# Performance work log

Measured on AMD Instinct MI355X. Metric: run time of the kernel, lower is better.

The kernel has to match this reference:

```python
import math
import jax, jax.numpy as jnp
import numpy as np

BS, N, D, H = 4, 512, 1024, 16
HD = D // H


def setup_inputs() -> dict:
    key = jax.random.key(0)
    ks = jax.random.split(key, 12)
    s = 1.0 / math.sqrt(D)
    return {
        "x": jax.random.normal(ks[0], (BS, N, D), jnp.float32),
        "r": jax.random.normal(ks[1], (BS, 3, N, N), jnp.float32),
        "bias": jax.random.normal(ks[2], (BS, H, N, N), jnp.float32),
        "mask": jax.random.randint(ks[3], (BS, 1, N, N), 0, 2, jnp.int32),
        "wq": jax.random.normal(ks[4], (D, D), jnp.float32) * s,
        "bq": jnp.zeros((D,), jnp.float32),
        "wk": jax.random.normal(ks[5], (D, D), jnp.float32) * s,
        "bk": jnp.zeros((D,), jnp.float32),
        "wv": jax.random.normal(ks[6], (D, D), jnp.float32) * s,
        "bv": jnp.zeros((D,), jnp.float32),
        "wo": jax.random.normal(ks[7], (D, 1), jnp.float32) * s,
        "bo": jnp.zeros((1,), jnp.float32),
    }


def reference(x, r, bias, mask, wq, bq, wk, bk, wv, bv, wo, bo):
    bs, n, d = x.shape
    # projections -> (bs, h, n, hd)
    q = (x @ wq + bq).reshape(bs, n, H, HD).transpose(0, 2, 1, 3)
    k = (x @ wk + bk).reshape(bs, n, H, HD).transpose(0, 2, 1, 3)
    v = (x @ wv + bv).reshape(bs, n, H, HD).transpose(0, 2, 1, 3)
    logits = jnp.einsum("bhid,bhjd->bhij", q, k) / math.sqrt(HD) + bias
    logits = jnp.where(mask == 0, jnp.float32(-1e9), logits)
    w = jax.nn.softmax(logits, axis=-1)  # (bs,h,n,n)
    # o[b,i,c,h,d] = sum_j r[b,c,i,j] * w[b,h,i,j] * v[b,h,j,d]
    o = jnp.einsum("bcij,bhij,bhjd->bichd", r, w, v)
    o = o.reshape(bs, n, 3, d)
    force = o @ wo + bo  # (bs, n, 3, 1)
    return force
```

## Files before the change

### kernel.cpp

```cpp
#include <hip/hip_runtime.h>
#include <stdint.h>

#define BSZ 4
#define NSEQ 512
#define DMOD 1024
#define NH 16
#define HD 64

typedef __attribute__((ext_vector_type(8))) short bf16x8;
typedef __attribute__((ext_vector_type(4))) float f32x4;

__device__ __forceinline__ unsigned short f2bf(float f) {
    union { float f; uint32_t u; } v; v.f = f;
    uint32_t u = v.u;
    u += 0x7FFFu + ((u >> 16) & 1u);
    return (unsigned short)(u >> 16);
}

__device__ __forceinline__ void gload_lds16(const unsigned short* g, unsigned short* l) {
    __builtin_amdgcn_global_load_lds(
        (const __attribute__((address_space(1))) void*)g,
        (__attribute__((address_space(3))) void*)l, 16, 0, 0);
}

#define LGKM_BAR() do { \
    asm volatile("s_waitcnt lgkmcnt(0)" ::: "memory"); \
    __builtin_amdgcn_sched_barrier(0); \
    __builtin_amdgcn_s_barrier(); \
    __builtin_amdgcn_sched_barrier(0); } while (0)

__global__ __launch_bounds__(256) void k_prep(
        const float* __restrict__ x, const float* __restrict__ wq, const float* __restrict__ wk,
        const float* __restrict__ wv, const float* __restrict__ bv, const float* __restrict__ wo,
        unsigned short* __restrict__ xb, unsigned short* __restrict__ wqt,
        unsigned short* __restrict__ wkt, float* __restrict__ wv2t, float* __restrict__ bv2) {
    __shared__ float t[32][33];
    int bx = blockIdx.x, tid = threadIdx.x;
    if (bx < 2048) {
        int i = bx * 256 + tid;
        float4 v = ((const float4*)x)[i];
        ushort4 o; o.x = f2bf(v.x); o.y = f2bf(v.y); o.z = f2bf(v.z); o.w = f2bf(v.w);
        ((ushort4*)xb)[i] = o;
    } else if (bx < 4096) {
        int g = bx - 2048; int z = g >> 10; g &= 1023;
        const float* src = z ? wk : wq;
        unsigned short* dst = z ? wkt : wqt;
        int be = (g & 31) * 32, bc = (g >> 5) * 32;
        int tx = tid & 31, ty = tid >> 5;
        #pragma unroll
        for (int yy = 0; yy < 32; yy += 8)
            t[ty + yy][tx] = src[(size_t)(be + ty + yy) * DMOD + bc + tx];
        __syncthreads();
        #pragma unroll
        for (int yy = 0; yy < 32; yy += 8)
            dst[(size_t)(bc + ty + yy) * DMOD + be + tx] = f2bf(t[tx][ty + yy]);
    } else {
        int g = bx - 4096;
        int grp = tid >> 6, l = tid & 63;
        int e = g * 4 + grp;
        float out = 0.f;
        #pragma unroll
        for (int it = 0; it < 16; ++it) {
            float v = wv[(size_t)e * DMOD + it * 64 + l] * wo[it * 64 + l];
            #pragma unroll
            for (int off = 1; off < 64; off <<= 1) v += __shfl_xor(v, off, 64);
            if (l == it) out = v;
        }
        if (l < 16) wv2t[l * DMOD + e] = out;
        if (g == 0 && grp == 0) {
            float ob = 0.f;
            #pragma unroll
            for (int it = 0; it < 16; ++it) {
                float v = bv[it * 64 + l] * wo[it * 64 + l];
                #pragma unroll
                for (int off = 1; off < 64; off <<= 1) v += __shfl_xor(v, off, 64);
                if (l == it) ob = v;
            }
            if (l < 16) bv2[l] = ob;
        }
    }
}

__global__ __launch_bounds__(256, 3) void k_mid(
        const float* __restrict__ x, const float* __restrict__ wv2t, const float* __restrict__ bv2,
        const unsigned short* __restrict__ xb, const unsigned short* __restrict__ wqt,
        const unsigned short* __restrict__ wkt, const float* __restrict__ bq,
        const float* __restrict__ bk, float* __restrict__ u,
        unsigned short* __restrict__ qT, unsigned short* __restrict__ kT) {
    __shared__ unsigned short lA[128 * 64];
    __shared__ unsigned short lB[128 * 64];
    int bx = blockIdx.x, tid = threadIdx.x;
    if (bx >= 256) {
        int wave = (bx - 256) * 4 + (tid >> 6);
        int l = tid & 63;
        int b = wave >> 9, j = wave & 511;
        const float* xr = x + (size_t)(b * NSEQ + j) * DMOD;
        float p[16];
        #pragma unroll
        for (int h = 0; h < 16; ++h) p[h] = 0.f;
        for (int it = 0; it < 16; ++it) {
            int e = l + it * 64;
            float xv = xr[e];
            #pragma unroll
            for (int h = 0; h < 16; ++h) p[h] += xv * wv2t[h * DMOD + e];
        }
        #pragma unroll
        for (int h = 0; h < 16; ++h) {
            #pragma unroll
            for (int off = 1; off < 64; off <<= 1) p[h] += __shfl_xor(p[h], off, 64);
        }
        float out = 0.f;
        #pragma unroll
        for (int h = 0; h < 16; ++h) if (l == h) out = p[h] + bv2[h];
        if (l < 16) u[(b * 16 + l) * NSEQ + j] = out;
        return;
    }
    int g = bx;
    int mt = g & 15, nt8 = (g >> 4) & 7, z = g >> 7;
    const unsigned short* Wt = z ? wkt : wqt;
    const float* bias = z ? bk : bq;
    unsigned short* outT = z ? kT : qT;
    float scale = z ? 1.f : 0.125f;
    int m0 = mt * 128, n0 = nt8 * 128;
    int w = tid >> 6, lane = tid & 63;
    int wr = w >> 1, wc = w & 1;
    int quad = lane >> 4, cs = lane & 15;
    int l8 = lane >> 3, l7 = lane & 7;
    int sg = l7 ^ l8;

    f32x4 acc[4][4];
    #pragma unroll
    for (int mi = 0; mi < 4; ++mi)
        #pragma unroll
        for (int ni = 0; ni < 4; ++ni) acc[mi][ni] = (f32x4){0.f, 0.f, 0.f, 0.f};

    for (int kc = 0; kc < 16; ++kc) {
        int k0 = kc * 64;
        #pragma unroll
        for (int q = 0; q < 4; ++q) {
            int row = w * 32 + q * 8 + l8;
            gload_lds16(xb + (size_t)(m0 + row) * DMOD + k0 + sg * 8,
                        &lA[(w * 32 + q * 8) * 64]);
            gload_lds16(Wt + (size_t)(n0 + row) * DMOD + k0 + sg * 8,
                        &lB[(w * 32 + q * 8) * 64]);
        }
        __syncthreads();
        #pragma unroll
        for (int ks = 0; ks < 2; ++ks) {
            bf16x8 af[4], bfr[4];
            #pragma unroll
            for (int mi = 0; mi < 4; ++mi) {
                int row = wr * 64 + mi * 16 + cs;
                int gq = (ks * 4 + quad) ^ (row & 7);
                af[mi] = *(const bf16x8*)&lA[row * 64 + gq * 8];
            }
            #pragma unroll
            for (int ni = 0; ni < 4; ++ni) {
                int row = wc * 64 + ni * 16 + cs;
                int gq = (ks * 4 + quad) ^ (row & 7);
                bfr[ni] = *(const bf16x8*)&lB[row * 64 + gq * 8];
            }
            #pragma unroll
            for (int mi = 0; mi < 4; ++mi)
                #pragma unroll
                for (int ni = 0; ni < 4; ++ni)
                    acc[mi][ni] = __builtin_amdgcn_mfma_f32_16x16x32_bf16(
                        af[mi], bfr[ni], acc[mi][ni], 0, 0, 0);
        }
        __syncthreads();
    }
    #pragma unroll
    for (int ni = 0; ni < 4; ++ni) {
        int n = n0 + wc * 64 + ni * 16 + cs;
        int h = n >> 6, d = n & 63;
        float bvv = bias[n];
        #pragma unroll
        for (int mi = 0; mi < 4; ++mi) {
            #pragma unroll
            for (int rr = 0; rr < 4; ++rr) {
                int mg = m0 + wr * 64 + mi * 16 + quad * 4 + rr;
                int b = mg >> 9, i = mg & 511;
                outT[(size_t)((b * 16 + h) * NSEQ + i) * HD + d] =
                    f2bf((acc[mi][ni][rr] + bvv) * scale);
            }
        }
    }
}

__global__ __launch_bounds__(512, 4) void k_attn(
        const unsigned short* __restrict__ qT, const unsigned short* __restrict__ kT,
        const float* __restrict__ bias, const int* __restrict__ mask,
        const float* __restrict__ u, const float* __restrict__ r,
        float* __restrict__ spart, float* __restrict__ P) {
    __shared__ float rT4[16 * 64 * 4];
    int tid = threadIdx.x;
    int w = tid >> 6, lane = tid & 63;
    int quad = lane >> 4, col = lane & 15;
    int it = blockIdx.x, jc = blockIdx.y, b = blockIdx.z;
    int i0 = it * 16, j0 = jc * 64;

    float s0[2], s1[2], s2[2], smf[2];
    const float* rbase = r + (size_t)b * 3 * NSEQ * NSEQ;
    const int* mrow = mask + (size_t)b * NSEQ * NSEQ;
    #pragma unroll
    for (int t = 0; t < 2; ++t) {
        int slot = t * 512 + tid;
        int il = slot >> 6, jl = slot & 63;
        size_t off = (size_t)(i0 + il) * NSEQ + j0 + jl;
        s0[t] = rbase[off];
        s1[t] = rbase[(size_t)NSEQ * NSEQ + off];
        s2[t] = rbase[2 * (size_t)NSEQ * NSEQ + off];
        smf[t] = (float)mrow[off];
    }
    #pragma unroll
    for (int t = 0; t < 2; ++t) {
        int slot = t * 512 + tid;
        float4 pk; pk.x = s0[t]; pk.y = s1[t]; pk.z = s2[t]; pk.w = smf[t];
        *(float4*)&rT4[slot * 4] = pk;
    }

    LGKM_BAR();

    #pragma unroll
    for (int hg = 0; hg < 2; ++hg) {
        int bh = b * 16 + hg * 8 + w;

        const unsigned short* qbase = qT + ((size_t)(bh * NSEQ + i0 + col)) * HD + quad * 8;
        bf16x8 a0 = *(const bf16x8*)qbase;
        bf16x8 a1 = *(const bf16x8*)(qbase + 32);

        bf16x8 kf0[4], kf1[4];
        #pragma unroll
        for (int jt = 0; jt < 4; ++jt) {
            const unsigned short* kbase =
                kT + ((size_t)(bh * NSEQ + j0 + jt * 16 + col)) * HD + quad * 8;
            kf0[jt] = *(const bf16x8*)kbase;
            kf1[jt] = *(const bf16x8*)(kbase + 32);
        }
        const float* brow = bias + (size_t)bh * NSEQ * NSEQ;
        float bvv[16];
        #pragma unroll
        for (int jt = 0; jt < 4; ++jt) {
            int j = j0 + jt * 16 + col;
            #pragma unroll
            for (int rr = 0; rr < 4; ++rr) {
                int i = i0 + quad * 4 + rr;
                bvv[jt * 4 + rr] = __builtin_nontemporal_load(&brow[(size_t)i * NSEQ + j]);
            }
        }
        const float* ub = u + (size_t)bh * NSEQ;
        float uvv[4];
        #pragma unroll
        for (int jt = 0; jt < 4; ++jt) uvv[jt] = ub[j0 + jt * 16 + col];

        float sp[4] = {0.f, 0.f, 0.f, 0.f};
        float pc0[4] = {0.f, 0.f, 0.f, 0.f};
        float pc1[4] = {0.f, 0.f, 0.f, 0.f};
        float pc2[4] = {0.f, 0.f, 0.f, 0.f};
        #pragma unroll
        for (int jt = 0; jt < 4; ++jt) {
            f32x4 acc = (f32x4){0.f, 0.f, 0.f, 0.f};
            acc = __builtin_amdgcn_mfma_f32_16x16x32_bf16(a0, kf0[jt], acc, 0, 0, 0);
            acc = __builtin_amdgcn_mfma_f32_16x16x32_bf16(a1, kf1[jt], acc, 0, 0, 0);
            float uv = uvv[jt];
            int jl = jt * 16 + col;
            #pragma unroll
            for (int rr = 0; rr < 4; ++rr) {
                int il = quad * 4 + rr;
                float4 v = *(const float4*)&rT4[(il * 64 + jl) * 4];
                float lg = acc[rr] + bvv[jt * 4 + rr];
                float e = __expf(lg) * v.w;
                sp[rr] += e;
                float eu = e * uv;
                pc0[rr] += eu * v.x;
                pc1[rr] += eu * v.y;
                pc2[rr] += eu * v.z;
            }
        }
        #pragma unroll
        for (int rr = 0; rr < 4; ++rr) {
            #pragma unroll
            for (int off = 1; off < 16; off <<= 1) {
                sp[rr]  += __shfl_xor(sp[rr], off, 64);
                pc0[rr] += __shfl_xor(pc0[rr], off, 64);
                pc1[rr] += __shfl_xor(pc1[rr], off, 64);
                pc2[rr] += __shfl_xor(pc2[rr], off, 64);
            }
        }
        if (col == 0) {
            #pragma unroll
            for (int rr = 0; rr < 4; ++rr) {
                int il = quad * 4 + rr;
                spart[((size_t)bh * NSEQ + i0 + il) * 8 + jc] = sp[rr];
                size_t pb = ((((size_t)bh * 32 + it) * 16 + il) * 8 + jc) * 3;
                P[pb + 0] = pc0[rr];
                P[pb + 1] = pc1[rr];
                P[pb + 2] = pc2[rr];
            }
        }
    }
}

__global__ __launch_bounds__(256) void k_final(
        const float* __restrict__ spart, const float* __restrict__ P,
        const float* __restrict__ bo, float* __restrict__ out) {
    __shared__ float part[4][16][3];
    int bx = blockIdx.x;
    int b = bx >> 5, it = bx & 31;
    int tid = threadIdx.x;
    int il = tid & 15, h = tid >> 4;
    int w = tid >> 6;
    int bh = b * 16 + h;
    int i = it * 16 + il;
    const float* sprow = spart + ((size_t)bh * NSEQ + i) * 8;
    float4 sa = *(const float4*)sprow;
    float4 sb = *(const float4*)(sprow + 4);
    float s = sa.x + sa.y + sa.z + sa.w + sb.x + sb.y + sb.z + sb.w;
    float sinv = (s > 0.f) ? 1.f / s : 0.f;
    const float* pbase = P + (((size_t)bh * 32 + it) * 16 + il) * 24;
    float f[3] = {0.f, 0.f, 0.f};
    #pragma unroll
    for (int q = 0; q < 6; ++q) {
        float4 v = *(const float4*)(pbase + q * 4);
        f[(q * 4 + 0) % 3] += v.x;
        f[(q * 4 + 1) % 3] += v.y;
        f[(q * 4 + 2) % 3] += v.z;
        f[(q * 4 + 3) % 3] += v.w;
    }
    f[0] *= sinv; f[1] *= sinv; f[2] *= sinv;
    #pragma unroll
    for (int c = 0; c < 3; ++c) {
        f[c] += __shfl_xor(f[c], 16, 64);
        f[c] += __shfl_xor(f[c], 32, 64);
    }
    if ((tid & 48) == 0) {
        part[w][il][0] = f[0]; part[w][il][1] = f[1]; part[w][il][2] = f[2];
    }
    __syncthreads();
    if (tid < 16) {
        float bov = bo[0];
        float o0 = part[0][tid][0] + part[1][tid][0] + part[2][tid][0] + part[3][tid][0];
        float o1 = part[0][tid][1] + part[1][tid][1] + part[2][tid][1] + part[3][tid][1];
        float o2 = part[0][tid][2] + part[1][tid][2] + part[2][tid][2] + part[3][tid][2];
        size_t row = (size_t)b * NSEQ + it * 16 + tid;
        out[row * 3 + 0] = o0 + bov;
        out[row * 3 + 1] = o1 + bov;
        out[row * 3 + 2] = o2 + bov;
    }
}

extern "C" void kernel_launch(void* const* d_in, const int* in_sizes, int n_in,
                              void* d_out, int out_size, void* d_ws, size_t ws_size,
                              hipStream_t stream) {
    const float* x    = (const float*)d_in[0];
    const float* rr   = (const float*)d_in[1];
    const float* bias = (const float*)d_in[2];
    const int*   mask = (const int*)d_in[3];
    const float* wq   = (const float*)d_in[4];
    const float* bq   = (const float*)d_in[5];
    const float* wk   = (const float*)d_in[6];
    const float* bk   = (const float*)d_in[7];
    const float* wv   = (const float*)d_in[8];
    const float* bv   = (const float*)d_in[9];
    const float* wo   = (const float*)d_in[10];
    const float* bo   = (const float*)d_in[11];
    float* out = (float*)d_out;

    char* ws = (char*)d_ws;
    unsigned short* xb    = (unsigned short*)(ws + 0);
    unsigned short* wqt   = (unsigned short*)(ws + 4194304);
    unsigned short* wkt   = (unsigned short*)(ws + 6291456);
    float*          wv2t  = (float*)(ws + 8388608);
    float*          bv2   = (float*)(ws + 8454144);
    float*          u     = (float*)(ws + 8454400);
    unsigned short* qT    = (unsigned short*)(ws + 8585472);
    unsigned short* kT    = (unsigned short*)(ws + 12779776);
    float*          spart = (float*)(ws + 16974080);
    float*          P     = (float*)(ws + 18022656);

    k_prep<<<4352, 256, 0, stream>>>(x, wq, wk, wv, bv, wo, xb, wqt, wkt, wv2t, bv2);
    k_mid<<<768, 256, 0, stream>>>(x, wv2t, bv2, xb, wqt, wkt, bq, bk, u, qT, kT);
    k_attn<<<dim3(32, 8, 4), 512, 0, stream>>>(qT, kT, bias, mask, u, rr, spart, P);
    k_final<<<128, 256, 0, stream>>>(spart, P, bo, out);
}
```

Baseline: 194.7 us.

## Split attention heads across grid and stream bias tile into LDS asynchronously

```diff
diff --git a/kernel.cpp b/kernel.cpp
--- a/kernel.cpp
+++ b/kernel.cpp
@@ -18,6 +18,12 @@
 }
 
 __device__ __forceinline__ void gload_lds16(const unsigned short* g, unsigned short* l) {
+    __builtin_amdgcn_global_load_lds(
+        (const __attribute__((address_space(1))) void*)g,
+        (__attribute__((address_space(3))) void*)l, 16, 0, 0);
+}
+
+__device__ __forceinline__ void gload_lds16f(const float* g, float* l) {
     __builtin_amdgcn_global_load_lds(
         (const __attribute__((address_space(1))) void*)g,
         (__attribute__((address_space(3))) void*)l, 16, 0, 0);
@@ -187,17 +193,23 @@
     }
 }
 
+#define BGRP 264
+#define BHEAD 1056
 __global__ __launch_bounds__(512, 4) void k_attn(
         const unsigned short* __restrict__ qT, const unsigned short* __restrict__ kT,
         const float* __restrict__ bias, const int* __restrict__ mask,
         const float* __restrict__ u, const float* __restrict__ r,
         float* __restrict__ spart, float* __restrict__ P) {
+    __shared__ float bias_lds[8 * BHEAD];
     __shared__ float rT4[16 * 64 * 4];
     int tid = threadIdx.x;
     int w = tid >> 6, lane = tid & 63;
     int quad = lane >> 4, col = lane & 15;
-    int it = blockIdx.x, jc = blockIdx.y, b = blockIdx.z;
+    int it = blockIdx.x, jc = blockIdx.y, bz = blockIdx.z;
+    int b = bz >> 1, hg = bz & 1;
     int i0 = it * 16, j0 = jc * 64;
+    int h = hg * 8 + w;
+    int bh = b * 16 + h;
 
     float s0[2], s1[2], s2[2], smf[2];
     const float* rbase = r + (size_t)b * 3 * NSEQ * NSEQ;
@@ -212,6 +224,32 @@
         s2[t] = rbase[2 * (size_t)NSEQ * NSEQ + off];
         smf[t] = (float)mrow[off];
     }
+
+    const unsigned short* qbase = qT + ((size_t)(bh * NSEQ + i0 + col)) * HD + quad * 8;
+    bf16x8 a0 = *(const bf16x8*)qbase;
+    bf16x8 a1 = *(const bf16x8*)(qbase + 32);
+    bf16x8 kf0[4], kf1[4];
+    #pragma unroll
+    for (int jt = 0; jt < 4; ++jt) {
+        const unsigned short* kbase =
+            kT + ((size_t)(bh * NSEQ + j0 + jt * 16 + col)) * HD + quad * 8;
+        kf0[jt] = *(const bf16x8*)kbase;
+        kf1[jt] = *(const bf16x8*)(kbase + 32);
+    }
+    const float* ub = u + (size_t)bh * NSEQ;
+    float uvv[4];
+    #pragma unroll
+    for (int jt = 0; jt < 4; ++jt) uvv[jt] = ub[j0 + jt * 16 + col];
+
+    {
+        const float* bsrc = bias + (size_t)bh * NSEQ * NSEQ;
+        int il4 = lane >> 4, jl4 = (lane & 15) * 4;
+        #pragma unroll
+        for (int g = 0; g < 4; ++g)
+            gload_lds16f(bsrc + (size_t)(i0 + g * 4 + il4) * NSEQ + j0 + jl4,
+                         &bias_lds[w * BHEAD + g * BGRP]);
+    }
+
     #pragma unroll
     for (int t = 0; t < 2; ++t) {
         int slot = t * 512 + tid;
@@ -220,83 +258,54 @@
     }
 
     LGKM_BAR();
-
-    #pragma unroll
-    for (int hg = 0; hg < 2; ++hg) {
-        int bh = b * 16 + hg * 8 + w;
-
-        const unsigned short* qbase = qT + ((size_t)(bh * NSEQ + i0 + col)) * HD + quad * 8;
-        bf16x8 a0 = *(const bf16x8*)qbase;
-        bf16x8 a1 = *(const bf16x8*)(qbase + 32);
-
-        bf16x8 kf0[4], kf1[4];
-        #pragma unroll
-        for (int jt = 0; jt < 4; ++jt) {
-            const unsigned short* kbase =
-                kT + ((size_t)(bh * NSEQ + j0 + jt * 16 + col)) * HD + quad * 8;
-            kf0[jt] = *(const bf16x8*)kbase;
-            kf1[jt] = *(const bf16x8*)(kbase + 32);
-        }
-        const float* brow = bias + (size_t)bh * NSEQ * NSEQ;
-        float bvv[16];
-        #pragma unroll
-        for (int jt = 0; jt < 4; ++jt) {
-            int j = j0 + jt * 16 + col;
-            #pragma unroll
-            for (int rr = 0; rr < 4; ++rr) {
-                int i = i0 + quad * 4 + rr;
-                bvv[jt * 4 + rr] = __builtin_nontemporal_load(&brow[(size_t)i * NSEQ + j]);
-            }
-        }
-        const float* ub = u + (size_t)bh * NSEQ;
-        float uvv[4];
-        #pragma unroll
-        for (int jt = 0; jt < 4; ++jt) uvv[jt] = ub[j0 + jt * 16 + col];
-
-        float sp[4] = {0.f, 0.f, 0.f, 0.f};
-        float pc0[4] = {0.f, 0.f, 0.f, 0.f};
-        float pc1[4] = {0.f, 0.f, 0.f, 0.f};
-        float pc2[4] = {0.f, 0.f, 0.f, 0.f};
-        #pragma unroll
-        for (int jt = 0; jt < 4; ++jt) {
-            f32x4 acc = (f32x4){0.f, 0.f, 0.f, 0.f};
-            acc = __builtin_amdgcn_mfma_f32_16x16x32_bf16(a0, kf0[jt], acc, 0, 0, 0);
-            acc = __builtin_amdgcn_mfma_f32_16x16x32_bf16(a1, kf1[jt], acc, 0, 0, 0);
-            float uv = uvv[jt];
-            int jl = jt * 16 + col;
-            #pragma unroll
-            for (int rr = 0; rr < 4; ++rr) {
-                int il = quad * 4 + rr;
-                float4 v = *(const float4*)&rT4[(il * 64 + jl) * 4];
-                float lg = acc[rr] + bvv[jt * 4 + rr];
-                float e = __expf(lg) * v.w;
-                sp[rr] += e;
-                float eu = e * uv;
-                pc0[rr] += eu * v.x;
-                pc1[rr] += eu * v.y;
-                pc2[rr] += eu * v.z;
-            }
-        }
+    asm volatile("s_waitcnt vmcnt(0)" ::: "memory");
+    __builtin_amdgcn_sched_barrier(0);
+
+    const float* bwave = &bias_lds[w * BHEAD];
+    float sp[4] = {0.f, 0.f, 0.f, 0.f};
+    float pc0[4] = {0.f, 0.f, 0.f, 0.f};
+    float pc1[4] = {0.f, 0.f, 0.f, 0.f};
+    float pc2[4] = {0.f, 0.f, 0.f, 0.f};
+    #pragma unroll
+    for (int jt = 0; jt < 4; ++jt) {
+        f32x4 acc = (f32x4){0.f, 0.f, 0.f, 0.f};
+        acc = __builtin_amdgcn_mfma_f32_16x16x32_bf16(a0, kf0[jt], acc, 0, 0, 0);
+        acc = __builtin_amdgcn_mfma_f32_16x16x32_bf16(a1, kf1[jt], acc, 0, 0, 0);
+        float uv = uvv[jt];
+        int jl = jt * 16 + col;
         #pragma unroll
         for (int rr = 0; rr < 4; ++rr) {
-            #pragma unroll
-            for (int off = 1; off < 16; off <<= 1) {
-                sp[rr]  += __shfl_xor(sp[rr], off, 64);
-                pc0[rr] += __shfl_xor(pc0[rr], off, 64);
-                pc1[rr] += __shfl_xor(pc1[rr], off, 64);
-                pc2[rr] += __shfl_xor(pc2[rr], off, 64);
-            }
-        }
-        if (col == 0) {
-            #pragma unroll
-            for (int rr = 0; rr < 4; ++rr) {
-                int il = quad * 4 + rr;
-                spart[((size_t)bh * NSEQ + i0 + il) * 8 + jc] = sp[rr];
-                size_t pb = ((((size_t)bh * 32 + it) * 16 + il) * 8 + jc) * 3;
-                P[pb + 0] = pc0[rr];
-                P[pb + 1] = pc1[rr];
-                P[pb + 2] = pc2[rr];
-            }
+            int il = quad * 4 + rr;
+            float4 v = *(const float4*)&rT4[(il * 64 + jl) * 4];
+            float bvv = bwave[quad * BGRP + rr * 64 + jl];
+            float lg = acc[rr] + bvv;
+            float e = __expf(lg) * v.w;
+            sp[rr] += e;
+            float eu = e * uv;
+            pc0[rr] += eu * v.x;
+            pc1[rr] += eu * v.y;
+            pc2[rr] += eu * v.z;
+        }
+    }
+    #pragma unroll
+    for (int rr = 0; rr < 4; ++rr) {
+        #pragma unroll
+        for (int off = 1; off < 16; off <<= 1) {
+            sp[rr]  += __shfl_xor(sp[rr], off, 64);
+            pc0[rr] += __shfl_xor(pc0[rr], off, 64);
+            pc1[rr] += __shfl_xor(pc1[rr], off, 64);
+            pc2[rr] += __shfl_xor(pc2[rr], off, 64);
+        }
+    }
+    if (col == 0) {
+        #pragma unroll
+        for (int rr = 0; rr < 4; ++rr) {
+            int il = quad * 4 + rr;
+            spart[((size_t)bh * NSEQ + i0 + il) * 8 + jc] = sp[rr];
+            size_t pb = ((((size_t)bh * 32 + it) * 16 + il) * 8 + jc) * 3;
+            P[pb + 0] = pc0[rr];
+            P[pb + 1] = pc1[rr];
+            P[pb + 2] = pc2[rr];
         }
     }
 }
@@ -380,6 +389,6 @@
 
     k_prep<<<4352, 256, 0, stream>>>(x, wq, wk, wv, bv, wo, xb, wqt, wkt, wv2t, bv2);
     k_mid<<<768, 256, 0, stream>>>(x, wv2t, bv2, xb, wqt, wkt, bq, bk, u, qT, kT);
-    k_attn<<<dim3(32, 8, 4), 512, 0, stream>>>(qT, kT, bias, mask, u, rr, spart, P);
+    k_attn<<<dim3(32, 8, 8), 512, 0, stream>>>(qT, kT, bias, mask, u, rr, spart, P);
     k_final<<<128, 256, 0, stream>>>(spart, P, bo, out);
 }
```

After: 186.7 us. -4.1%, faster.

## Restructure attention kernel to loop over key chunks with double-buffered prefetch

Applied to the files above, without the earlier changes.

```diff
diff --git a/kernel.cpp b/kernel.cpp
--- a/kernel.cpp
+++ b/kernel.cpp
@@ -187,88 +187,96 @@
     }
 }
 
-__global__ __launch_bounds__(512, 4) void k_attn(
+__global__ __launch_bounds__(512, 2) void k_attn(
         const unsigned short* __restrict__ qT, const unsigned short* __restrict__ kT,
         const float* __restrict__ bias, const int* __restrict__ mask,
         const float* __restrict__ u, const float* __restrict__ r,
         float* __restrict__ spart, float* __restrict__ P) {
-    __shared__ float rT4[16 * 64 * 4];
+    __shared__ float rT4[2][16 * 64 * 4];
     int tid = threadIdx.x;
     int w = tid >> 6, lane = tid & 63;
     int quad = lane >> 4, col = lane & 15;
-    int it = blockIdx.x, jc = blockIdx.y, b = blockIdx.z;
-    int i0 = it * 16, j0 = jc * 64;
-
-    float s0[2], s1[2], s2[2], smf[2];
+    int it = blockIdx.x, bz = blockIdx.y;
+    int b = bz >> 1, hg = bz & 1;
+    int i0 = it * 16;
+    int h = hg * 8 + w;
+    int bh = b * 16 + h;
+
     const float* rbase = r + (size_t)b * 3 * NSEQ * NSEQ;
     const int* mrow = mask + (size_t)b * NSEQ * NSEQ;
-    #pragma unroll
-    for (int t = 0; t < 2; ++t) {
-        int slot = t * 512 + tid;
-        int il = slot >> 6, jl = slot & 63;
-        size_t off = (size_t)(i0 + il) * NSEQ + j0 + jl;
-        s0[t] = rbase[off];
-        s1[t] = rbase[(size_t)NSEQ * NSEQ + off];
-        s2[t] = rbase[2 * (size_t)NSEQ * NSEQ + off];
-        smf[t] = (float)mrow[off];
-    }
-    #pragma unroll
-    for (int t = 0; t < 2; ++t) {
-        int slot = t * 512 + tid;
-        float4 pk; pk.x = s0[t]; pk.y = s1[t]; pk.z = s2[t]; pk.w = smf[t];
-        *(float4*)&rT4[slot * 4] = pk;
-    }
-
-    LGKM_BAR();
-
-    #pragma unroll
-    for (int hg = 0; hg < 2; ++hg) {
-        int bh = b * 16 + hg * 8 + w;
-
-        const unsigned short* qbase = qT + ((size_t)(bh * NSEQ + i0 + col)) * HD + quad * 8;
-        bf16x8 a0 = *(const bf16x8*)qbase;
-        bf16x8 a1 = *(const bf16x8*)(qbase + 32);
-
-        bf16x8 kf0[4], kf1[4];
+    const float* brow = bias + (size_t)bh * NSEQ * NSEQ;
+    const unsigned short* kbh = kT + (size_t)bh * NSEQ * HD;
+    const float* ub = u + (size_t)bh * NSEQ;
+
+    const unsigned short* qbase = qT + ((size_t)(bh * NSEQ + i0 + col)) * HD + quad * 8;
+    bf16x8 a0 = *(const bf16x8*)qbase;
+    bf16x8 a1 = *(const bf16x8*)(qbase + 32);
+
+    bf16x8 kf0[2][4], kf1[2][4];
+    float uvv[2][4], bvv[2][16];
+    float s0[2][2], s1[2][2], s2[2][2], smf[2][2];
+
+    auto prefetch = [&](int jc, int pb) {
+        int j0 = jc * 64;
         #pragma unroll
         for (int jt = 0; jt < 4; ++jt) {
-            const unsigned short* kbase =
-                kT + ((size_t)(bh * NSEQ + j0 + jt * 16 + col)) * HD + quad * 8;
-            kf0[jt] = *(const bf16x8*)kbase;
-            kf1[jt] = *(const bf16x8*)(kbase + 32);
-        }
-        const float* brow = bias + (size_t)bh * NSEQ * NSEQ;
-        float bvv[16];
-        #pragma unroll
-        for (int jt = 0; jt < 4; ++jt) {
+            const unsigned short* kb = kbh + ((size_t)(j0 + jt * 16 + col)) * HD + quad * 8;
+            kf0[pb][jt] = *(const bf16x8*)kb;
+            kf1[pb][jt] = *(const bf16x8*)(kb + 32);
+            uvv[pb][jt] = ub[j0 + jt * 16 + col];
             int j = j0 + jt * 16 + col;
             #pragma unroll
             for (int rr = 0; rr < 4; ++rr) {
                 int i = i0 + quad * 4 + rr;
-                bvv[jt * 4 + rr] = __builtin_nontemporal_load(&brow[(size_t)i * NSEQ + j]);
-            }
-        }
-        const float* ub = u + (size_t)bh * NSEQ;
-        float uvv[4];
-        #pragma unroll
-        for (int jt = 0; jt < 4; ++jt) uvv[jt] = ub[j0 + jt * 16 + col];
-
-        float sp[4] = {0.f, 0.f, 0.f, 0.f};
+                bvv[pb][jt * 4 + rr] = __builtin_nontemporal_load(&brow[(size_t)i * NSEQ + j]);
+            }
+        }
+        #pragma unroll
+        for (int t = 0; t < 2; ++t) {
+            int slot = t * 512 + tid;
+            int il = slot >> 6, jl = slot & 63;
+            size_t off = (size_t)(i0 + il) * NSEQ + j0 + jl;
+            s0[pb][t] = rbase[off];
+            s1[pb][t] = rbase[(size_t)NSEQ * NSEQ + off];
+            s2[pb][t] = rbase[2 * (size_t)NSEQ * NSEQ + off];
+            smf[pb][t] = (float)mrow[off];
+        }
+    };
+    auto pack = [&](int pb) {
+        #pragma unroll
+        for (int t = 0; t < 2; ++t) {
+            int slot = t * 512 + tid;
+            float4 pk; pk.x = s0[pb][t]; pk.y = s1[pb][t]; pk.z = s2[pb][t]; pk.w = smf[pb][t];
+            *(float4*)&rT4[pb][slot * 4] = pk;
+        }
+    };
+
+    prefetch(0, 0);
+    pack(0);
+    LGKM_BAR();
+
+    #pragma unroll 8
+    for (int jc = 0; jc < 8; ++jc) {
+        int cur = jc & 1, nxt = cur ^ 1;
+        if (jc < 7) prefetch(jc + 1, nxt);
+
+        float sp[4]  = {0.f, 0.f, 0.f, 0.f};
         float pc0[4] = {0.f, 0.f, 0.f, 0.f};
         float pc1[4] = {0.f, 0.f, 0.f, 0.f};
         float pc2[4] = {0.f, 0.f, 0.f, 0.f};
+        const float* rbuf = rT4[cur];
         #pragma unroll
         for (int jt = 0; jt < 4; ++jt) {
             f32x4 acc = (f32x4){0.f, 0.f, 0.f, 0.f};
-            acc = __builtin_amdgcn_mfma_f32_16x16x32_bf16(a0, kf0[jt], acc, 0, 0, 0);
-            acc = __builtin_amdgcn_mfma_f32_16x16x32_bf16(a1, kf1[jt], acc, 0, 0, 0);
-            float uv = uvv[jt];
+            acc = __builtin_amdgcn_mfma_f32_16x16x32_bf16(a0, kf0[cur][jt], acc, 0, 0, 0);
+            acc = __builtin_amdgcn_mfma_f32_16x16x32_bf16(a1, kf1[cur][jt], acc, 0, 0, 0);
+            float uv = uvv[cur][jt];
             int jl = jt * 16 + col;
             #pragma unroll
             for (int rr = 0; rr < 4; ++rr) {
                 int il = quad * 4 + rr;
-                float4 v = *(const float4*)&rT4[(il * 64 + jl) * 4];
-                float lg = acc[rr] + bvv[jt * 4 + rr];
+                float4 v = *(const float4*)&rbuf[(il * 64 + jl) * 4];
+                float lg = acc[rr] + bvv[cur][jt * 4 + rr];
                 float e = __expf(lg) * v.w;
                 sp[rr] += e;
                 float eu = e * uv;
@@ -292,12 +300,13 @@
             for (int rr = 0; rr < 4; ++rr) {
                 int il = quad * 4 + rr;
                 spart[((size_t)bh * NSEQ + i0 + il) * 8 + jc] = sp[rr];
-                size_t pb = ((((size_t)bh * 32 + it) * 16 + il) * 8 + jc) * 3;
-                P[pb + 0] = pc0[rr];
-                P[pb + 1] = pc1[rr];
-                P[pb + 2] = pc2[rr];
-            }
-        }
+                size_t pb2 = ((((size_t)bh * 32 + it) * 16 + il) * 8 + jc) * 3;
+                P[pb2 + 0] = pc0[rr];
+                P[pb2 + 1] = pc1[rr];
+                P[pb2 + 2] = pc2[rr];
+            }
+        }
+        if (jc < 7) { pack(nxt); LGKM_BAR(); }
     }
 }
 
@@ -380,6 +389,6 @@
 
     k_prep<<<4352, 256, 0, stream>>>(x, wq, wk, wv, bv, wo, xb, wqt, wkt, wv2t, bv2);
     k_mid<<<768, 256, 0, stream>>>(x, wv2t, bv2, xb, wqt, wkt, bq, bk, u, qT, kT);
-    k_attn<<<dim3(32, 8, 4), 512, 0, stream>>>(qT, kT, bias, mask, u, rr, spart, P);
+    k_attn<<<dim3(32, 8), 512, 0, stream>>>(qT, kT, bias, mask, u, rr, spart, P);
     k_final<<<128, 256, 0, stream>>>(spart, P, bo, out);
 }
```

Result: no change. 196.2 us (+0.8%).
